# Optimization experiments

Hardware: AMD Instinct MI355X
Metric: run time of the kernel (lower is better)

## Reference

```python
import jax, jax.numpy as jnp
import numpy as np

N_NODES = 100000
N_EDGES = 1600000
D_IN = 64
D_HID = 64
D_OUT = 64


def sage_conv(x, src, dst, W_l, W_r, b, n_nodes):
    # PyG SAGEConv (aggr='mean'): out = lin_l(mean_{j in N(i)} x_j) + lin_r(x_i)
    msg = x[src]                                   # [E, d] gather (irregular)
    agg = jax.ops.segment_sum(msg, dst, num_segments=n_nodes)   # [N, d]
    cnt = jax.ops.segment_sum(jnp.ones((src.shape[0], 1), x.dtype), dst,
                              num_segments=n_nodes)             # [N, 1]
    mean = agg / jnp.maximum(cnt, 1.0)
    return mean @ W_l + x @ W_r + b


def setup_inputs() -> dict:
    key = jax.random.key(0)
    k_x, k_e, k1, k2, k3, k4 = jax.random.split(key, 6)
    x = jax.random.normal(k_x, (N_NODES, D_IN), dtype=jnp.float32)
    edge_index = jax.random.randint(k_e, (2, N_EDGES), 0, N_NODES, dtype=jnp.int64)
    s = 1.0 / np.sqrt(D_IN)
    W_l1 = jax.random.uniform(k1, (D_IN, D_HID), jnp.float32, -s, s)
    W_r1 = jax.random.uniform(k2, (D_IN, D_HID), jnp.float32, -s, s)
    b1 = jnp.zeros((D_HID,), jnp.float32)
    s2 = 1.0 / np.sqrt(D_HID)
    W_l2 = jax.random.uniform(k3, (D_HID, D_OUT), jnp.float32, -s2, s2)
    W_r2 = jax.random.uniform(k4, (D_HID, D_OUT), jnp.float32, -s2, s2)
    b2 = jnp.zeros((D_OUT,), jnp.float32)
    return {"x": x, "edge_index": edge_index,
            "W_l1": W_l1, "W_r1": W_r1, "b1": b1,
            "W_l2": W_l2, "W_r2": W_r2, "b2": b2}


def reference(x, edge_index, W_l1, W_r1, b1, W_l2, W_r2, b2):
    src, dst = edge_index[0], edge_index[1]
    n = x.shape[0]
    h = sage_conv(x, src, dst, W_l1, W_r1, b1, n)
    h = jax.nn.relu(h)
    # dropout is identity in eval mode (training=False)
    out = sage_conv(h, src, dst, W_l2, W_r2, b2, n)
    return out
```

## Files before the change

kernel.cpp:

```cpp
#include <hip/hip_runtime.h>

#define DFEAT 64
#define SBSH 10
#define SBN 1024
#define NSB 98
#define ETILE 4096
#define PACKSH 17
#define SRCMASK 0x1FFFF

typedef __bf16 bf16x8 __attribute__((ext_vector_type(8)));
typedef float f32x4 __attribute__((ext_vector_type(4)));

__device__ __forceinline__ unsigned bf16_rne(float v) {
    unsigned bits = __float_as_uint(v);
    return (bits + 0x7FFFu + ((bits >> 16) & 1u)) >> 16;
}

__global__ __launch_bounds__(512) void bhist_kernel(const int* __restrict__ dst,
                                                    int n_edges, int nt,
                                                    int* __restrict__ counts) {
    __shared__ int lh[NSB];
    int t = threadIdx.x;
    if (t < NSB) lh[t] = 0;
    __syncthreads();
    int s0 = blockIdx.x * ETILE;
    int s1 = s0 + ETILE; if (s1 > n_edges) s1 = n_edges;
    for (int e = s0 + t; e < s1; e += 512)
        atomicAdd(&lh[dst[e] >> SBSH], 1);
    __syncthreads();
    if (t < NSB) counts[t * nt + blockIdx.x] = lh[t];
}

__global__ __launch_bounds__(512) void tscan1_kernel(const int* __restrict__ counts,
                                                     int nt,
                                                     int* __restrict__ tilebase,
                                                     int* __restrict__ sbtot) {
    __shared__ int sdata[512];
    int sb = blockIdx.x, t = threadIdx.x;
    int v = (t < nt) ? counts[sb * nt + t] : 0;
    sdata[t] = v;
    __syncthreads();
    for (int off = 1; off < 512; off <<= 1) {
        int x = (t >= off) ? sdata[t - off] : 0;
        __syncthreads();
        sdata[t] += x;
        __syncthreads();
    }
    if (t < nt) tilebase[sb * nt + t] = sdata[t] - v;
    if (t == 511) sbtot[sb] = sdata[511];
}

__global__ __launch_bounds__(128) void tscan2_kernel(const int* __restrict__ sbtot,
                                                     int* __restrict__ sbbase,
                                                     int n_edges) {
    __shared__ int sdata[128];
    int t = threadIdx.x;
    int v = (t < NSB) ? sbtot[t] : 0;
    sdata[t] = v;
    __syncthreads();
    for (int off = 1; off < 128; off <<= 1) {
        int x = (t >= off) ? sdata[t - off] : 0;
        __syncthreads();
        sdata[t] += x;
        __syncthreads();
    }
    if (t < NSB) sbbase[t] = sdata[t] - v;
    if (t == 0) sbbase[NSB] = n_edges;
}

__global__ __launch_bounds__(512) void partition_kernel(const int* __restrict__ src,
                                                        const int* __restrict__ dst,
                                                        int n_edges, int nt,
                                                        const int* __restrict__ tilebase,
                                                        const int* __restrict__ sbbase,
                                                        int* __restrict__ tmp) {
    __shared__ int lcur[NSB];
    int t = threadIdx.x;
    if (t < NSB) lcur[t] = sbbase[t] + tilebase[t * nt + blockIdx.x];
    __syncthreads();
    int s0 = blockIdx.x * ETILE;
    int s1 = s0 + ETILE; if (s1 > n_edges) s1 = n_edges;
    for (int e = s0 + t; e < s1; e += 512) {
        int d = dst[e];
        int sb = d >> SBSH;
        int ofs = atomicAdd(&lcur[sb], 1);
        tmp[ofs] = ((d & (SBN - 1)) << PACKSH) | src[e];
    }
}

__global__ __launch_bounds__(1024) void bucket_sort_kernel(
    const int* __restrict__ sbbase, const int* __restrict__ tmp,
    int* __restrict__ col_src, int* __restrict__ row_ptr,
    int n_nodes, int n_edges) {
    __shared__ int cnt[SBN];
    __shared__ int scan[SBN];
    int b = blockIdx.x, t = threadIdx.x;
    int gb = sbbase[b], ge = sbbase[b + 1];
    cnt[t] = 0;
    __syncthreads();
    for (int e = gb + t; e < ge; e += 1024)
        atomicAdd(&cnt[((unsigned)tmp[e]) >> PACKSH], 1);
    __syncthreads();
    int v = cnt[t];
    scan[t] = v;
    __syncthreads();
    for (int off = 1; off < 1024; off <<= 1) {
        int x = (t >= off) ? scan[t - off] : 0;
        __syncthreads();
        scan[t] += x;
        __syncthreads();
    }
    int excl = scan[t] - v;
    int node = (b << SBSH) + t;
    if (node < n_nodes) row_ptr[node] = gb + excl;
    cnt[t] = gb + excl;
    if (b == (int)gridDim.x - 1 && t == 0) row_ptr[n_nodes] = n_edges;
    __syncthreads();
    for (int e = gb + t; e < ge; e += 1024) {
        int pk = tmp[e];
        int pos = atomicAdd(&cnt[((unsigned)pk) >> PACKSH], 1);
        col_src[pos] = (pk & SRCMASK) << 7;
    }
}

__global__ __launch_bounds__(256) void cvt_kernel(const float* __restrict__ x,
                                                  unsigned short* __restrict__ xb,
                                                  int n8) {
    int i = blockIdx.x * 256 + threadIdx.x;
    if (i >= n8) return;
    const float4* xp = (const float4*)x;
    float4 a = xp[2 * i], c = xp[2 * i + 1];
    int4 o;
    o.x = bf16_rne(a.x) | (bf16_rne(a.y) << 16);
    o.y = bf16_rne(a.z) | (bf16_rne(a.w) << 16);
    o.z = bf16_rne(c.x) | (bf16_rne(c.y) << 16);
    o.w = bf16_rne(c.z) | (bf16_rne(c.w) << 16);
    ((int4*)xb)[i] = o;
}

__global__ __launch_bounds__(256) void wpack_kernel(
    const float* __restrict__ Wl1, const float* __restrict__ Wr1,
    const float* __restrict__ Wl2, const float* __restrict__ Wr2,
    unsigned short* __restrict__ wpack) {
    int u = blockIdx.x * 256 + threadIdx.x;
    if (u >= 2048) return;
    int l = u & 63;
    int ct = (u >> 6) & 3;
    int chunk = (u >> 8) & 1;
    int gemm = (u >> 9) & 1;
    int layer = (u >> 10) & 1;
    const float* W = layer ? (gemm ? Wr2 : Wl2) : (gemm ? Wr1 : Wl1);
    int col = ct * 16 + (l & 15);
    int k0 = chunk * 32 + (l >> 4) * 8;
    unsigned hi[8], lo[8];
#pragma unroll
    for (int j = 0; j < 8; ++j) {
        float w = W[(k0 + j) * DFEAT + col];
        unsigned h = bf16_rne(w);
        float whi = __uint_as_float(h << 16);
        lo[j] = bf16_rne(w - whi);
        hi[j] = h;
    }
    size_t fh = ((((size_t)(layer * 2 + gemm) * 2 + 0) * 2 + chunk) * 4 + ct) * 64 + l;
    size_t fl = ((((size_t)(layer * 2 + gemm) * 2 + 1) * 2 + chunk) * 4 + ct) * 64 + l;
    int4 vh, vl;
    vh.x = hi[0] | (hi[1] << 16); vh.y = hi[2] | (hi[3] << 16);
    vh.z = hi[4] | (hi[5] << 16); vh.w = hi[6] | (hi[7] << 16);
    vl.x = lo[0] | (lo[1] << 16); vl.y = lo[2] | (lo[3] << 16);
    vl.z = lo[4] | (lo[5] << 16); vl.w = lo[6] | (lo[7] << 16);
    ((int4*)wpack)[fh] = vh;
    ((int4*)wpack)[fl] = vl;
}

__global__ __launch_bounds__(512, 8) void agg_kernel(
    const int* __restrict__ row_ptr, const int* __restrict__ col_src,
    const unsigned short* __restrict__ xb, unsigned short* __restrict__ meanb,
    int n_nodes) {
    int w = threadIdx.x >> 6;
    int lane = threadIdx.x & 63;
    int g = lane >> 3;
    int p = lane & 7;
    int node = blockIdx.x * 8 + w;
    if (node >= n_nodes) return;

    int start = row_ptr[node];
    int end = row_ptr[node + 1];
    int deg = end - start;

    float acc[8] = {0.f, 0.f, 0.f, 0.f, 0.f, 0.f, 0.f, 0.f};
    const char* xbase = (const char*)xb + p * 16;

    for (int base = start; base < end; base += 64) {
        int m = end - base; if (m > 64) m = 64;
        int soff = col_src[base + (lane < m ? lane : 0)];
        for (int i = 0; i < m; i += 32) {
#pragma unroll
            for (int k = 0; k < 4; ++k) {
                if (i + 8 * k < m) {
                    int n = i + 8 * k + g;
                    int off = __shfl(soff, n < m ? n : 0);
                    float f = (n < m) ? 1.0f : 0.0f;
                    int4 v = *(const int4*)(xbase + off);
                    acc[0] += f * __uint_as_float(((unsigned)v.x) << 16);
                    acc[1] += f * __uint_as_float(((unsigned)v.x) & 0xFFFF0000u);
                    acc[2] += f * __uint_as_float(((unsigned)v.y) << 16);
                    acc[3] += f * __uint_as_float(((unsigned)v.y) & 0xFFFF0000u);
                    acc[4] += f * __uint_as_float(((unsigned)v.z) << 16);
                    acc[5] += f * __uint_as_float(((unsigned)v.z) & 0xFFFF0000u);
                    acc[6] += f * __uint_as_float(((unsigned)v.w) << 16);
                    acc[7] += f * __uint_as_float(((unsigned)v.w) & 0xFFFF0000u);
                }
            }
        }
    }

#pragma unroll
    for (int d = 8; d < 64; d <<= 1) {
#pragma unroll
        for (int e = 0; e < 8; ++e) acc[e] += __shfl_xor(acc[e], d);
    }

    if (g == 0) {
        float inv = (deg > 0) ? 1.0f / (float)deg : 0.0f;
        unsigned u[8];
#pragma unroll
        for (int e = 0; e < 8; ++e) u[e] = bf16_rne(acc[e] * inv);
        int4 o;
        o.x = u[0] | (u[1] << 16);
        o.y = u[2] | (u[3] << 16);
        o.z = u[4] | (u[5] << 16);
        o.w = u[6] | (u[7] << 16);
        *(int4*)((char*)meanb + (size_t)node * 128 + p * 16) = o;
    }
}

template <bool RELU, bool OUT_BF16>
__global__ __launch_bounds__(256) void linear_kernel(
    const unsigned short* __restrict__ Ab, const unsigned short* __restrict__ Xb,
    const unsigned short* __restrict__ wpack,
    const float* __restrict__ bias, void* __restrict__ outp,
    int n_nodes, int ntiles) {
    int wave = (blockIdx.x * 256 + threadIdx.x) >> 6;
    if (wave >= ntiles) return;
    int l = threadIdx.x & 63;
    int row16 = l & 15;
    int kq = l >> 4;
    int node0 = wave * 16;

    int arow = node0 + row16;
    if (arow >= n_nodes) arow = n_nodes - 1;
    const char* ap = (const char*)Ab + (size_t)arow * 128 + kq * 16;
    const char* xp = (const char*)Xb + (size_t)arow * 128 + kq * 16;
    bf16x8 aA0 = *(const bf16x8*)ap;
    bf16x8 aA1 = *(const bf16x8*)(ap + 64);
    bf16x8 aX0 = *(const bf16x8*)xp;
    bf16x8 aX1 = *(const bf16x8*)(xp + 64);

    const bf16x8* wp = (const bf16x8*)wpack;
#pragma unroll
    for (int ct = 0; ct < 4; ++ct) {
        float bcol = bias[ct * 16 + row16];
        f32x4 acc = {bcol, bcol, bcol, bcol};
        bf16x8 b000 = wp[0 * 256 + ct * 64 + l];
        bf16x8 b001 = wp[1 * 256 + ct * 64 + l];
        bf16x8 b010 = wp[2 * 256 + ct * 64 + l];
        bf16x8 b011 = wp[3 * 256 + ct * 64 + l];
        bf16x8 b100 = wp[4 * 256 + ct * 64 + l];
        bf16x8 b101 = wp[5 * 256 + ct * 64 + l];
        bf16x8 b110 = wp[6 * 256 + ct * 64 + l];
        bf16x8 b111 = wp[7 * 256 + ct * 64 + l];
        acc = __builtin_amdgcn_mfma_f32_16x16x32_bf16(aA0, b000, acc, 0, 0, 0);
        acc = __builtin_amdgcn_mfma_f32_16x16x32_bf16(aA1, b001, acc, 0, 0, 0);
        acc = __builtin_amdgcn_mfma_f32_16x16x32_bf16(aA0, b010, acc, 0, 0, 0);
        acc = __builtin_amdgcn_mfma_f32_16x16x32_bf16(aA1, b011, acc, 0, 0, 0);
        acc = __builtin_amdgcn_mfma_f32_16x16x32_bf16(aX0, b100, acc, 0, 0, 0);
        acc = __builtin_amdgcn_mfma_f32_16x16x32_bf16(aX1, b101, acc, 0, 0, 0);
        acc = __builtin_amdgcn_mfma_f32_16x16x32_bf16(aX0, b110, acc, 0, 0, 0);
        acc = __builtin_amdgcn_mfma_f32_16x16x32_bf16(aX1, b111, acc, 0, 0, 0);
#pragma unroll
        for (int reg = 0; reg < 4; ++reg) {
            int row = kq * 4 + reg;
            int gn = node0 + row;
            if (gn < n_nodes) {
                float v = acc[reg];
                if (RELU) v = fmaxf(v, 0.0f);
                if (OUT_BF16) {
                    ((unsigned short*)outp)[(size_t)gn * DFEAT + ct * 16 + row16] =
                        (unsigned short)bf16_rne(v);
                } else {
                    ((float*)outp)[(size_t)gn * DFEAT + ct * 16 + row16] = v;
                }
            }
        }
    }
}

extern "C" void kernel_launch(void* const* d_in, const int* in_sizes, int n_in,
                              void* d_out, int out_size, void* d_ws, size_t ws_size,
                              hipStream_t stream) {
    const float* x   = (const float*)d_in[0];
    const int*   ei  = (const int*)d_in[1];
    const float* Wl1 = (const float*)d_in[2];
    const float* Wr1 = (const float*)d_in[3];
    const float* b1  = (const float*)d_in[4];
    const float* Wl2 = (const float*)d_in[5];
    const float* Wr2 = (const float*)d_in[6];
    const float* b2  = (const float*)d_in[7];
    float* out = (float*)d_out;

    int n_nodes = in_sizes[0] / DFEAT;
    int n_edges = in_sizes[1] / 2;
    const int* src  = ei;
    const int* dstv = ei + n_edges;
    int nt = (n_edges + ETILE - 1) / ETILE;

    auto align = [](size_t v) { return (v + 255) & ~(size_t)255; };
    char* ws = (char*)d_ws;
    int* counts   = (int*)ws;            ws += align((size_t)NSB * nt * 4);
    int* tilebase = (int*)ws;            ws += align((size_t)NSB * nt * 4);
    int* sbtot    = (int*)ws;            ws += align(NSB * 4);
    int* sbbase   = (int*)ws;            ws += align((NSB + 1) * 4);
    int* row_ptr  = (int*)ws;            ws += align(((size_t)n_nodes + 1) * 4);
    int* col_src  = (int*)ws;            ws += align((size_t)n_edges * 4);
    unsigned short* xb    = (unsigned short*)ws; ws += align((size_t)n_nodes * DFEAT * 2);
    unsigned short* hb    = (unsigned short*)ws; ws += align((size_t)n_nodes * DFEAT * 2);
    unsigned short* meanb = (unsigned short*)ws; ws += align((size_t)n_nodes * DFEAT * 2);
    unsigned short* wpack = (unsigned short*)ws; ws += align((size_t)32768);
    int* tmp      = (int*)d_out;

    bhist_kernel<<<nt, 512, 0, stream>>>(dstv, n_edges, nt, counts);
    tscan1_kernel<<<NSB, 512, 0, stream>>>(counts, nt, tilebase, sbtot);
    tscan2_kernel<<<1, 128, 0, stream>>>(sbtot, sbbase, n_edges);
    partition_kernel<<<nt, 512, 0, stream>>>(src, dstv, n_edges, nt, tilebase,
                                             sbbase, tmp);
    bucket_sort_kernel<<<NSB, 1024, 0, stream>>>(sbbase, tmp, col_src, row_ptr,
                                                 n_nodes, n_edges);

    int n8 = n_nodes * DFEAT / 8;
    cvt_kernel<<<(n8 + 255) / 256, 256, 0, stream>>>(x, xb, n8);
    wpack_kernel<<<8, 256, 0, stream>>>(Wl1, Wr1, Wl2, Wr2, wpack);

    int ntiles = (n_nodes + 15) / 16;
    int nb = (n_nodes + 7) / 8;
    int lb = (ntiles + 3) / 4;

    agg_kernel<<<nb, 512, 0, stream>>>(row_ptr, col_src, xb, meanb, n_nodes);
    linear_kernel<true, true><<<lb, 256, 0, stream>>>(meanb, xb, wpack, b1,
                                                      hb, n_nodes, ntiles);
    agg_kernel<<<nb, 512, 0, stream>>>(row_ptr, col_src, hb, meanb, n_nodes);
    linear_kernel<false, false><<<lb, 256, 0, stream>>>(meanb, hb, wpack + 2048 * 8,
                                                        b2, out, n_nodes, ntiles);
}
```

Measured before the change: 169.6 us.

## Fuse aggregation with MFMA linear layer and merge setup kernels

Fuses the mean-aggregation and the linear MFMA stage into a single per-16-node-tile kernel. The mean rows stay in shared memory, so the meanb round trip through global memory and two launches go away. Each wave now aggregates two nodes, with 16 lanes per neighbor row using 8-byte loads. The histogram, weight-pack and x-conversion kernels are merged into one launch. In exchange, only 4 of 8 waves run the MFMA phase, and imbalance between the paired nodes' degrees can leave lanes idle.

```diff
diff --git a/kernel.cpp b/kernel.cpp
--- a/kernel.cpp
+++ b/kernel.cpp
@@ -15,20 +15,67 @@
     unsigned bits = __float_as_uint(v);
     return (bits + 0x7FFFu + ((bits >> 16) & 1u)) >> 16;
 }
-
-__global__ __launch_bounds__(512) void bhist_kernel(const int* __restrict__ dst,
-                                                    int n_edges, int nt,
-                                                    int* __restrict__ counts) {
-    __shared__ int lh[NSB];
-    int t = threadIdx.x;
-    if (t < NSB) lh[t] = 0;
-    __syncthreads();
-    int s0 = blockIdx.x * ETILE;
-    int s1 = s0 + ETILE; if (s1 > n_edges) s1 = n_edges;
-    for (int e = s0 + t; e < s1; e += 512)
-        atomicAdd(&lh[dst[e] >> SBSH], 1);
-    __syncthreads();
-    if (t < NSB) counts[t * nt + blockIdx.x] = lh[t];
+__device__ __forceinline__ float lo16(unsigned u) { return __uint_as_float(u << 16); }
+__device__ __forceinline__ float hi16(unsigned u) { return __uint_as_float(u & 0xFFFF0000u); }
+
+__global__ __launch_bounds__(512) void setup_kernel(
+    const int* __restrict__ dst, int n_edges, int nt, int* __restrict__ counts,
+    const float* __restrict__ x, unsigned short* __restrict__ xb, int ncvt,
+    const float* __restrict__ Wl1, const float* __restrict__ Wr1,
+    const float* __restrict__ Wl2, const float* __restrict__ Wr2,
+    unsigned short* __restrict__ wpack) {
+    int b = blockIdx.x, t = threadIdx.x;
+    if (b < nt) {
+        __shared__ int lh[NSB];
+        if (t < NSB) lh[t] = 0;
+        __syncthreads();
+        int s0 = b * ETILE;
+        int s1 = s0 + ETILE; if (s1 > n_edges) s1 = n_edges;
+        for (int e = s0 + t; e < s1; e += 512)
+            atomicAdd(&lh[dst[e] >> SBSH], 1);
+        __syncthreads();
+        if (t < NSB) counts[t * nt + b] = lh[t];
+    } else if (b < nt + 4) {
+        int u = (b - nt) * 512 + t;
+        int l = u & 63;
+        int ct = (u >> 6) & 3;
+        int chunk = (u >> 8) & 1;
+        int gemm = (u >> 9) & 1;
+        int layer = (u >> 10) & 1;
+        const float* W = layer ? (gemm ? Wr2 : Wl2) : (gemm ? Wr1 : Wl1);
+        int col = ct * 16 + (l & 15);
+        int k0 = chunk * 32 + (l >> 4) * 8;
+        unsigned hi[8], lo[8];
+#pragma unroll
+        for (int j = 0; j < 8; ++j) {
+            float w = W[(k0 + j) * DFEAT + col];
+            unsigned h = bf16_rne(w);
+            float whi = __uint_as_float(h << 16);
+            lo[j] = bf16_rne(w - whi);
+            hi[j] = h;
+        }
+        size_t fh = ((((size_t)(layer * 2 + gemm) * 2 + 0) * 2 + chunk) * 4 + ct) * 64 + l;
+        size_t fl = ((((size_t)(layer * 2 + gemm) * 2 + 1) * 2 + chunk) * 4 + ct) * 64 + l;
+        int4 vh, vl;
+        vh.x = hi[0] | (hi[1] << 16); vh.y = hi[2] | (hi[3] << 16);
+        vh.z = hi[4] | (hi[5] << 16); vh.w = hi[6] | (hi[7] << 16);
+        vl.x = lo[0] | (lo[1] << 16); vl.y = lo[2] | (lo[3] << 16);
+        vl.z = lo[4] | (lo[5] << 16); vl.w = lo[6] | (lo[7] << 16);
+        ((int4*)wpack)[fh] = vh;
+        ((int4*)wpack)[fl] = vl;
+    } else {
+        int i = (b - nt - 4) * 512 + t;
+        if (i < ncvt) {
+            const float4* xp = (const float4*)x;
+            float4 a = xp[2 * i], c = xp[2 * i + 1];
+            int4 o;
+            o.x = bf16_rne(a.x) | (bf16_rne(a.y) << 16);
+            o.y = bf16_rne(a.z) | (bf16_rne(a.w) << 16);
+            o.z = bf16_rne(c.x) | (bf16_rne(c.y) << 16);
+            o.w = bf16_rne(c.z) | (bf16_rne(c.w) << 16);
+            ((int4*)xb)[i] = o;
+        }
+    }
 }
 
 __global__ __launch_bounds__(512) void tscan1_kernel(const int* __restrict__ counts,
@@ -123,160 +170,108 @@
     }
 }
 
-__global__ __launch_bounds__(256) void cvt_kernel(const float* __restrict__ x,
-                                                  unsigned short* __restrict__ xb,
-                                                  int n8) {
-    int i = blockIdx.x * 256 + threadIdx.x;
-    if (i >= n8) return;
-    const float4* xp = (const float4*)x;
-    float4 a = xp[2 * i], c = xp[2 * i + 1];
-    int4 o;
-    o.x = bf16_rne(a.x) | (bf16_rne(a.y) << 16);
-    o.y = bf16_rne(a.z) | (bf16_rne(a.w) << 16);
-    o.z = bf16_rne(c.x) | (bf16_rne(c.y) << 16);
-    o.w = bf16_rne(c.z) | (bf16_rne(c.w) << 16);
-    ((int4*)xb)[i] = o;
-}
-
-__global__ __launch_bounds__(256) void wpack_kernel(
-    const float* __restrict__ Wl1, const float* __restrict__ Wr1,
-    const float* __restrict__ Wl2, const float* __restrict__ Wr2,
-    unsigned short* __restrict__ wpack) {
-    int u = blockIdx.x * 256 + threadIdx.x;
-    if (u >= 2048) return;
-    int l = u & 63;
-    int ct = (u >> 6) & 3;
-    int chunk = (u >> 8) & 1;
-    int gemm = (u >> 9) & 1;
-    int layer = (u >> 10) & 1;
-    const float* W = layer ? (gemm ? Wr2 : Wl2) : (gemm ? Wr1 : Wl1);
-    int col = ct * 16 + (l & 15);
-    int k0 = chunk * 32 + (l >> 4) * 8;
-    unsigned hi[8], lo[8];
-#pragma unroll
-    for (int j = 0; j < 8; ++j) {
-        float w = W[(k0 + j) * DFEAT + col];
-        unsigned h = bf16_rne(w);
-        float whi = __uint_as_float(h << 16);
-        lo[j] = bf16_rne(w - whi);
-        hi[j] = h;
-    }
-    size_t fh = ((((size_t)(layer * 2 + gemm) * 2 + 0) * 2 + chunk) * 4 + ct) * 64 + l;
-    size_t fl = ((((size_t)(layer * 2 + gemm) * 2 + 1) * 2 + chunk) * 4 + ct) * 64 + l;
-    int4 vh, vl;
-    vh.x = hi[0] | (hi[1] << 16); vh.y = hi[2] | (hi[3] << 16);
-    vh.z = hi[4] | (hi[5] << 16); vh.w = hi[6] | (hi[7] << 16);
-    vl.x = lo[0] | (lo[1] << 16); vl.y = lo[2] | (lo[3] << 16);
-    vl.z = lo[4] | (lo[5] << 16); vl.w = lo[6] | (lo[7] << 16);
-    ((int4*)wpack)[fh] = vh;
-    ((int4*)wpack)[fl] = vl;
-}
-
-__global__ __launch_bounds__(512, 8) void agg_kernel(
+template <bool RELU, bool OUT_BF16>
+__global__ __launch_bounds__(512, 4) void sage_kernel(
     const int* __restrict__ row_ptr, const int* __restrict__ col_src,
-    const unsigned short* __restrict__ xb, unsigned short* __restrict__ meanb,
-    int n_nodes) {
-    int w = threadIdx.x >> 6;
-    int lane = threadIdx.x & 63;
-    int g = lane >> 3;
-    int p = lane & 7;
-    int node = blockIdx.x * 8 + w;
-    if (node >= n_nodes) return;
-
-    int start = row_ptr[node];
-    int end = row_ptr[node + 1];
-    int deg = end - start;
-
-    float acc[8] = {0.f, 0.f, 0.f, 0.f, 0.f, 0.f, 0.f, 0.f};
-    const char* xbase = (const char*)xb + p * 16;
-
-    for (int base = start; base < end; base += 64) {
-        int m = end - base; if (m > 64) m = 64;
-        int soff = col_src[base + (lane < m ? lane : 0)];
-        for (int i = 0; i < m; i += 32) {
+    const unsigned short* __restrict__ xb,
+    const unsigned short* __restrict__ wpk,
+    const float* __restrict__ bias, void* __restrict__ outp, int n_nodes) {
+    __shared__ unsigned short sMean[16 * 72];
+    int t = threadIdx.x;
+    int w = t >> 6;
+    int lane = t & 63;
+    int g4 = lane >> 4;
+    int p4 = lane & 15;
+    int node0 = blockIdx.x * 16;
+    const char* xb8 = (const char*)xb + p4 * 8;
+
+    int nA = node0 + w;
+    int nB = node0 + w + 8;
+    int ncA = nA < n_nodes ? nA : n_nodes - 1;
+    int ncB = nB < n_nodes ? nB : n_nodes - 1;
+    int baseA = row_ptr[ncA], endA = row_ptr[ncA + 1];
+    int baseB = row_ptr[ncB], endB = row_ptr[ncB + 1];
+    int degA = endA - baseA, degB = endB - baseB;
+
+    float accA[4] = {0.f, 0.f, 0.f, 0.f};
+    float accB[4] = {0.f, 0.f, 0.f, 0.f};
+
+    while (baseA < endA || baseB < endB) {
+        int mA = endA - baseA; if (mA > 64) mA = 64; if (mA < 0) mA = 0;
+        int mB = endB - baseB; if (mB > 64) mB = 64; if (mB < 0) mB = 0;
+        int soffA = mA > 0 ? col_src[baseA + (lane < mA ? lane : 0)] : 0;
+        int soffB = mB > 0 ? col_src[baseB + (lane < mB ? lane : 0)] : 0;
+        int mmax = mA > mB ? mA : mB;
+        for (int i = 0; i < mmax; i += 16) {
 #pragma unroll
             for (int k = 0; k < 4; ++k) {
-                if (i + 8 * k < m) {
-                    int n = i + 8 * k + g;
-                    int off = __shfl(soff, n < m ? n : 0);
-                    float f = (n < m) ? 1.0f : 0.0f;
-                    int4 v = *(const int4*)(xbase + off);
-                    acc[0] += f * __uint_as_float(((unsigned)v.x) << 16);
-                    acc[1] += f * __uint_as_float(((unsigned)v.x) & 0xFFFF0000u);
-                    acc[2] += f * __uint_as_float(((unsigned)v.y) << 16);
-                    acc[3] += f * __uint_as_float(((unsigned)v.y) & 0xFFFF0000u);
-                    acc[4] += f * __uint_as_float(((unsigned)v.z) << 16);
-                    acc[5] += f * __uint_as_float(((unsigned)v.z) & 0xFFFF0000u);
-                    acc[6] += f * __uint_as_float(((unsigned)v.w) << 16);
-                    acc[7] += f * __uint_as_float(((unsigned)v.w) & 0xFFFF0000u);
+                int base4 = i + 4 * k;
+                int n = base4 + g4;
+                if (base4 < mA) {
+                    int off = __shfl(soffA, n < mA ? n : 0);
+                    float f = (n < mA) ? 1.f : 0.f;
+                    int2 v = *(const int2*)(xb8 + off);
+                    accA[0] += f * lo16((unsigned)v.x);
+                    accA[1] += f * hi16((unsigned)v.x);
+                    accA[2] += f * lo16((unsigned)v.y);
+                    accA[3] += f * hi16((unsigned)v.y);
+                }
+                if (base4 < mB) {
+                    int off = __shfl(soffB, n < mB ? n : 0);
+                    float f = (n < mB) ? 1.f : 0.f;
+                    int2 v = *(const int2*)(xb8 + off);
+                    accB[0] += f * lo16((unsigned)v.x);
+                    accB[1] += f * hi16((unsigned)v.x);
+                    accB[2] += f * lo16((unsigned)v.y);
+                    accB[3] += f * hi16((unsigned)v.y);
                 }
             }
         }
+        baseA += 64;
+        baseB += 64;
     }
 
 #pragma unroll
-    for (int d = 8; d < 64; d <<= 1) {
-#pragma unroll
-        for (int e = 0; e < 8; ++e) acc[e] += __shfl_xor(acc[e], d);
-    }
-
-    if (g == 0) {
-        float inv = (deg > 0) ? 1.0f / (float)deg : 0.0f;
-        unsigned u[8];
-#pragma unroll
-        for (int e = 0; e < 8; ++e) u[e] = bf16_rne(acc[e] * inv);
-        int4 o;
-        o.x = u[0] | (u[1] << 16);
-        o.y = u[2] | (u[3] << 16);
-        o.z = u[4] | (u[5] << 16);
-        o.w = u[6] | (u[7] << 16);
-        *(int4*)((char*)meanb + (size_t)node * 128 + p * 16) = o;
-    }
-}
-
-template <bool RELU, bool OUT_BF16>
-__global__ __launch_bounds__(256) void linear_kernel(
-    const unsigned short* __restrict__ Ab, const unsigned short* __restrict__ Xb,
-    const unsigned short* __restrict__ wpack,
-    const float* __restrict__ bias, void* __restrict__ outp,
-    int n_nodes, int ntiles) {
-    int wave = (blockIdx.x * 256 + threadIdx.x) >> 6;
-    if (wave >= ntiles) return;
-    int l = threadIdx.x & 63;
-    int row16 = l & 15;
-    int kq = l >> 4;
-    int node0 = wave * 16;
-
-    int arow = node0 + row16;
-    if (arow >= n_nodes) arow = n_nodes - 1;
-    const char* ap = (const char*)Ab + (size_t)arow * 128 + kq * 16;
-    const char* xp = (const char*)Xb + (size_t)arow * 128 + kq * 16;
-    bf16x8 aA0 = *(const bf16x8*)ap;
-    bf16x8 aA1 = *(const bf16x8*)(ap + 64);
-    bf16x8 aX0 = *(const bf16x8*)xp;
-    bf16x8 aX1 = *(const bf16x8*)(xp + 64);
-
-    const bf16x8* wp = (const bf16x8*)wpack;
-#pragma unroll
-    for (int ct = 0; ct < 4; ++ct) {
+    for (int e = 0; e < 4; ++e) {
+        accA[e] += __shfl_xor(accA[e], 16); accA[e] += __shfl_xor(accA[e], 32);
+        accB[e] += __shfl_xor(accB[e], 16); accB[e] += __shfl_xor(accB[e], 32);
+    }
+
+    if (g4 == 0) {
+        float invA = degA > 0 ? 1.f / (float)degA : 0.f;
+        float invB = degB > 0 ? 1.f / (float)degB : 0.f;
+        int2 oA, oB;
+        oA.x = bf16_rne(accA[0] * invA) | (bf16_rne(accA[1] * invA) << 16);
+        oA.y = bf16_rne(accA[2] * invA) | (bf16_rne(accA[3] * invA) << 16);
+        oB.x = bf16_rne(accB[0] * invB) | (bf16_rne(accB[1] * invB) << 16);
+        oB.y = bf16_rne(accB[2] * invB) | (bf16_rne(accB[3] * invB) << 16);
+        *(int2*)&sMean[w * 72 + p4 * 4] = oA;
+        *(int2*)&sMean[(w + 8) * 72 + p4 * 4] = oB;
+    }
+    __syncthreads();
+
+    if (w < 4) {
+        int ct = w;
+        int row16 = lane & 15;
+        int kq = lane >> 4;
+        bf16x8 aA0 = *(const bf16x8*)&sMean[row16 * 72 + kq * 8];
+        bf16x8 aA1 = *(const bf16x8*)&sMean[row16 * 72 + 32 + kq * 8];
+        int xr = node0 + row16; if (xr >= n_nodes) xr = n_nodes - 1;
+        const char* xp = (const char*)xb + (size_t)xr * 128 + kq * 16;
+        bf16x8 aX0 = *(const bf16x8*)xp;
+        bf16x8 aX1 = *(const bf16x8*)(xp + 64);
+
+        const bf16x8* wp = (const bf16x8*)wpk;
         float bcol = bias[ct * 16 + row16];
         f32x4 acc = {bcol, bcol, bcol, bcol};
-        bf16x8 b000 = wp[0 * 256 + ct * 64 + l];
-        bf16x8 b001 = wp[1 * 256 + ct * 64 + l];
-        bf16x8 b010 = wp[2 * 256 + ct * 64 + l];
-        bf16x8 b011 = wp[3 * 256 + ct * 64 + l];
-        bf16x8 b100 = wp[4 * 256 + ct * 64 + l];
-        bf16x8 b101 = wp[5 * 256 + ct * 64 + l];
-        bf16x8 b110 = wp[6 * 256 + ct * 64 + l];
-        bf16x8 b111 = wp[7 * 256 + ct * 64 + l];
-        acc = __builtin_amdgcn_mfma_f32_16x16x32_bf16(aA0, b000, acc, 0, 0, 0);
-        acc = __builtin_amdgcn_mfma_f32_16x16x32_bf16(aA1, b001, acc, 0, 0, 0);
-        acc = __builtin_amdgcn_mfma_f32_16x16x32_bf16(aA0, b010, acc, 0, 0, 0);
-        acc = __builtin_amdgcn_mfma_f32_16x16x32_bf16(aA1, b011, acc, 0, 0, 0);
-        acc = __builtin_amdgcn_mfma_f32_16x16x32_bf16(aX0, b100, acc, 0, 0, 0);
-        acc = __builtin_amdgcn_mfma_f32_16x16x32_bf16(aX1, b101, acc, 0, 0, 0);
-        acc = __builtin_amdgcn_mfma_f32_16x16x32_bf16(aX0, b110, acc, 0, 0, 0);
-        acc = __builtin_amdgcn_mfma_f32_16x16x32_bf16(aX1, b111, acc, 0, 0, 0);
+        acc = __builtin_amdgcn_mfma_f32_16x16x32_bf16(aA0, wp[0 * 256 + ct * 64 + lane], acc, 0, 0, 0);
+        acc = __builtin_amdgcn_mfma_f32_16x16x32_bf16(aA1, wp[1 * 256 + ct * 64 + lane], acc, 0, 0, 0);
+        acc = __builtin_amdgcn_mfma_f32_16x16x32_bf16(aA0, wp[2 * 256 + ct * 64 + lane], acc, 0, 0, 0);
+        acc = __builtin_amdgcn_mfma_f32_16x16x32_bf16(aA1, wp[3 * 256 + ct * 64 + lane], acc, 0, 0, 0);
+        acc = __builtin_amdgcn_mfma_f32_16x16x32_bf16(aX0, wp[4 * 256 + ct * 64 + lane], acc, 0, 0, 0);
+        acc = __builtin_amdgcn_mfma_f32_16x16x32_bf16(aX1, wp[5 * 256 + ct * 64 + lane], acc, 0, 0, 0);
+        acc = __builtin_amdgcn_mfma_f32_16x16x32_bf16(aX0, wp[6 * 256 + ct * 64 + lane], acc, 0, 0, 0);
+        acc = __builtin_amdgcn_mfma_f32_16x16x32_bf16(aX1, wp[7 * 256 + ct * 64 + lane], acc, 0, 0, 0);
 #pragma unroll
         for (int reg = 0; reg < 4; ++reg) {
             int row = kq * 4 + reg;
@@ -324,11 +319,14 @@
     int* col_src  = (int*)ws;            ws += align((size_t)n_edges * 4);
     unsigned short* xb    = (unsigned short*)ws; ws += align((size_t)n_nodes * DFEAT * 2);
     unsigned short* hb    = (unsigned short*)ws; ws += align((size_t)n_nodes * DFEAT * 2);
-    unsigned short* meanb = (unsigned short*)ws; ws += align((size_t)n_nodes * DFEAT * 2);
     unsigned short* wpack = (unsigned short*)ws; ws += align((size_t)32768);
     int* tmp      = (int*)d_out;
 
-    bhist_kernel<<<nt, 512, 0, stream>>>(dstv, n_edges, nt, counts);
+    int ncvt = n_nodes * DFEAT / 8;
+    int cvtb = (ncvt + 511) / 512;
+    setup_kernel<<<nt + 4 + cvtb, 512, 0, stream>>>(dstv, n_edges, nt, counts,
+                                                    x, xb, ncvt,
+                                                    Wl1, Wr1, Wl2, Wr2, wpack);
     tscan1_kernel<<<NSB, 512, 0, stream>>>(counts, nt, tilebase, sbtot);
     tscan2_kernel<<<1, 128, 0, stream>>>(sbtot, sbbase, n_edges);
     partition_kernel<<<nt, 512, 0, stream>>>(src, dstv, n_edges, nt, tilebase,
@@ -336,18 +334,10 @@
     bucket_sort_kernel<<<NSB, 1024, 0, stream>>>(sbbase, tmp, col_src, row_ptr,
                                                  n_nodes, n_edges);
 
-    int n8 = n_nodes * DFEAT / 8;
-    cvt_kernel<<<(n8 + 255) / 256, 256, 0, stream>>>(x, xb, n8);
-    wpack_kernel<<<8, 256, 0, stream>>>(Wl1, Wr1, Wl2, Wr2, wpack);
-
-    int ntiles = (n_nodes + 15) / 16;
-    int nb = (n_nodes + 7) / 8;
-    int lb = (ntiles + 3) / 4;
-
-    agg_kernel<<<nb, 512, 0, stream>>>(row_ptr, col_src, xb, meanb, n_nodes);
-    linear_kernel<true, true><<<lb, 256, 0, stream>>>(meanb, xb, wpack, b1,
-                                                      hb, n_nodes, ntiles);
-    agg_kernel<<<nb, 512, 0, stream>>>(row_ptr, col_src, hb, meanb, n_nodes);
-    linear_kernel<false, false><<<lb, 256, 0, stream>>>(meanb, hb, wpack + 2048 * 8,
-                                                        b2, out, n_nodes, ntiles);
-}
+    int tiles = (n_nodes + 15) / 16;
+    sage_kernel<true, true><<<tiles, 512, 0, stream>>>(row_ptr, col_src, xb,
+                                                       wpack, b1, hb, n_nodes);
+    sage_kernel<false, false><<<tiles, 512, 0, stream>>>(row_ptr, col_src, hb,
+                                                         wpack + 2048 * 8, b2,
+                                                         out, n_nodes);
+}
```

New measurement: 151.5 us. 10.7% less time.
